# Kernel tuning notes

Hardware: AMD Instinct MI355X
Metric: run time of the kernel (lower is better)

Reference implementation:

```python
import jax, jax.numpy as jnp
import numpy as np

WS = 8        # window size (square)
HEADS = 8
DIM = 512
EPS = 1e-5


def _ln(x, g, b):
    m = x.mean(-1, keepdims=True)
    v = x.var(-1, keepdims=True)
    return (x - m) / jnp.sqrt(v + EPS) * g + b


def _bn(x, g, b, m, v):
    # eval-mode BatchNorm2d on NCHW
    sh = (1, -1, 1, 1)
    return (x - m.reshape(sh)) / jnp.sqrt(v.reshape(sh) + EPS) * g.reshape(sh) + b.reshape(sh)


def _win_rev(w, H, W, C):
    # (B*nW, WS*WS, C) -> (B, C, H, W)
    x = w.reshape(-1, H // WS, W // WS, WS, WS, C)
    return x.transpose(0, 5, 1, 3, 2, 4).reshape(-1, C, H, W)


def _win_part(x):
    # (B, C, H, W) -> (B*nW, WS*WS, C)
    B, C, H, W = x.shape
    x = x.reshape(B, C, H // WS, WS, W // WS, WS)
    return x.transpose(0, 2, 4, 3, 5, 1).reshape(-1, WS * WS, C)


def setup_inputs() -> dict:
    key = jax.random.key(0)
    ks = iter(jax.random.split(key, 64))
    def nrm(sh, s=0.02):
        return jax.random.normal(next(ks), sh, jnp.float32) * s
    C, C2, C8 = DIM, DIM // 2, DIM // 8
    B, H, W = 2, 224, 224
    N = WS * WS
    B_ = B * (H // WS) * (W // WS)
    # relative position index (same construction as the torch module)
    coords = np.stack(np.meshgrid(np.arange(WS), np.arange(WS), indexing='ij'))
    cf = coords.reshape(2, -1)
    rel = (cf[:, :, None] - cf[:, None, :]).transpose(1, 2, 0).astype(np.int64)
    rel[:, :, 0] += WS - 1
    rel[:, :, 1] += WS - 1
    rel[:, :, 0] *= 2 * WS - 1
    rel_idx = jnp.asarray(rel.sum(-1), jnp.int32)   # (N, N)
    ones = lambda n: jnp.ones((n,), jnp.float32)
    zeros = lambda n: jnp.zeros((n,), jnp.float32)
    return dict(
        x=jax.random.normal(next(ks), (B_, N, C), jnp.float32),
        w_pa=nrm((C, C2)), b_pa=zeros(C2),
        g_lna=ones(C2) + nrm((C2,), 0.1), b_lna=nrm((C2,), 0.1),
        w_pc=nrm((C, C)), b_pc=zeros(C),
        g_lnc=ones(C) + nrm((C,), 0.1), b_lnc=nrm((C,), 0.1),
        dw_w=nrm((C, 1, 3, 3), 0.1), dw_b=zeros(C),
        g_bn1=ones(C), b_bn1=zeros(C), m_bn1=nrm((C,), 0.1), v_bn1=ones(C),
        ci_w1=nrm((C, C8)), ci_b1=zeros(C8),
        g_bn2=ones(C8), b_bn2=zeros(C8), m_bn2=nrm((C8,), 0.1), v_bn2=ones(C8),
        ci_w2=nrm((C8, C2)), ci_b2=zeros(C2),
        pj_w=nrm((C, C2)), pj_b=zeros(C2),
        g_bn3=ones(C2), b_bn3=zeros(C2), m_bn3=nrm((C2,), 0.1), v_bn3=ones(C2),
        w_qkv=nrm((C2, 3 * C2)), b_qkv=zeros(3 * C2),
        si_w1=nrm((C2, C8)), si_b1=zeros(C8),
        g_bn4=ones(C8), b_bn4=zeros(C8), m_bn4=nrm((C8,), 0.1), v_bn4=ones(C8),
        si_w2=nrm((C8, 1)), si_b2=zeros(1),
        g_lno=ones(C2) + nrm((C2,), 0.1), b_lno=nrm((C2,), 0.1),
        w_out=nrm((C, C)), b_out=zeros(C),
        rpb=nrm(((2 * WS - 1) ** 2, HEADS)),
        rel_idx=rel_idx, H=H, W=W,
    )


def _forward(x, w_pa, b_pa, g_lna, b_lna, w_pc, b_pc, g_lnc, b_lnc,
             dw_w, dw_b, g_bn1, b_bn1, m_bn1, v_bn1,
             ci_w1, ci_b1, g_bn2, b_bn2, m_bn2, v_bn2, ci_w2, ci_b2,
             pj_w, pj_b, g_bn3, b_bn3, m_bn3, v_bn3,
             w_qkv, b_qkv,
             si_w1, si_b1, g_bn4, b_bn4, m_bn4, v_bn4, si_w2, si_b2,
             g_lno, b_lno, w_out, b_out, rpb, rel_idx, H, W):
    B_, N, C = x.shape
    C2 = C // 2
    hd = C2 // HEADS
    scale = hd ** -0.5
    x_att = _ln(x @ w_pa + b_pa, g_lna, b_lna)            # (B_, N, C2)
    x_cnn = _ln(x @ w_pc + b_pc, g_lnc, b_lnc)            # (B_, N, C)
    x_cnn = _win_rev(x_cnn, H, W, C)                      # (B, C, H, W)
    # depthwise 3x3 conv + BN + GELU
    x_cnn = jax.lax.conv_general_dilated(
        x_cnn, dw_w, (1, 1), [(1, 1), (1, 1)],
        feature_group_count=C, dimension_numbers=('NCHW', 'OIHW', 'NCHW')
    ) + dw_b.reshape(1, -1, 1, 1)
    x_cnn = jax.nn.gelu(_bn(x_cnn, g_bn1, b_bn1, m_bn1, v_bn1), approximate=False)
    # channel interaction: global avg pool -> 1x1 conv -> BN -> GELU -> 1x1 conv
    ci = x_cnn.mean((2, 3))                               # (B, C)
    ci = ci @ ci_w1 + ci_b1                               # (B, C/8)
    ci = jax.nn.gelu((ci - m_bn2) / jnp.sqrt(v_bn2 + EPS) * g_bn2 + b_bn2, approximate=False)
    ci = ci @ ci_w2 + ci_b2                               # (B, C2)
    x_cnn = jnp.einsum('bchw,co->bohw', x_cnn, pj_w) + pj_b.reshape(1, -1, 1, 1)  # (B, C2, H, W)
    # windowed multi-head attention
    qkv = (x_att @ w_qkv + b_qkv).reshape(B_, N, 3, HEADS, hd).transpose(2, 0, 3, 1, 4)
    q, k, v = qkv[0], qkv[1], qkv[2]                      # (B_, heads, N, hd)
    B = ci.shape[0]
    gate = jax.nn.sigmoid(ci).reshape(B, 1, HEADS, 1, hd)
    v = (v.reshape(B, -1, HEADS, N, hd) * gate).reshape(B_, HEADS, N, hd)
    attn = jnp.einsum('bhnd,bhmd->bhnm', q * scale, k)    # (B_, heads, N, N)
    bias = rpb[rel_idx[:N, :N].reshape(-1)].reshape(N, N, HEADS).transpose(2, 0, 1)
    attn = jax.nn.softmax(attn + bias[None], axis=-1)
    x_att = jnp.einsum('bhnm,bhmd->bnhd', attn, v).reshape(B_, N, C2)
    # spatial interaction gating of the conv branch
    x_sp = _win_rev(x_att, H, W, C2)                      # (B, C2, H, W)
    si = jnp.einsum('bchw,co->bohw', x_sp, si_w1) + si_b1.reshape(1, -1, 1, 1)
    si = jax.nn.gelu(_bn(si, g_bn4, b_bn4, m_bn4, v_bn4), approximate=False)
    si = jnp.einsum('bchw,co->bohw', si, si_w2) + si_b2.reshape(1, -1, 1, 1)      # (B, 1, H, W)
    x_cnn = _bn(jax.nn.sigmoid(si) * x_cnn, g_bn3, b_bn3, m_bn3, v_bn3)
    x_cnn = _win_part(x_cnn)                              # (B_, N, C2)
    x_att = _ln(x_att, g_lno, b_lno)
    return jnp.concatenate([x_att, x_cnn], axis=-1) @ w_out + b_out


def reference(x, w_pa, b_pa, g_lna, b_lna, w_pc, b_pc, g_lnc, b_lnc,
              dw_w, dw_b, g_bn1, b_bn1, m_bn1, v_bn1,
              ci_w1, ci_b1, g_bn2, b_bn2, m_bn2, v_bn2, ci_w2, ci_b2,
              pj_w, pj_b, g_bn3, b_bn3, m_bn3, v_bn3,
              w_qkv, b_qkv,
              si_w1, si_b1, g_bn4, b_bn4, m_bn4, v_bn4, si_w2, si_b2,
              g_lno, b_lno, w_out, b_out, rpb, rel_idx, H, W):
    return _forward(x, w_pa, b_pa, g_lna, b_lna, w_pc, b_pc, g_lnc, b_lnc,
                    dw_w, dw_b, g_bn1, b_bn1, m_bn1, v_bn1,
                    ci_w1, ci_b1, g_bn2, b_bn2, m_bn2, v_bn2, ci_w2, ci_b2,
                    pj_w, pj_b, g_bn3, b_bn3, m_bn3, v_bn3,
                    w_qkv, b_qkv,
                    si_w1, si_b1, g_bn4, b_bn4, m_bn4, v_bn4, si_w2, si_b2,
                    g_lno, b_lno, w_out, b_out, rpb, rel_idx, H, W)
```

## Files before the change

### kernel.cpp

```cpp
#include <hip/hip_runtime.h>
#include <math.h>

#define EPS 1e-5f
#define MROWS 100352
#define NWIN  1568

typedef __attribute__((ext_vector_type(8))) short bf16x8;
typedef __attribute__((ext_vector_type(4))) float f32x4;

__device__ __forceinline__ unsigned short f2bf(float f) {
  unsigned u = __float_as_uint(f);
  u += 0x7fffu + ((u >> 16) & 1u);
  return (unsigned short)(u >> 16);
}
__device__ __forceinline__ float bf2f(unsigned short s) {
  return __uint_as_float(((unsigned)s) << 16);
}
__device__ __forceinline__ float gelu_exact(float x) {
  return 0.5f * x * (1.f + erff(x * 0.70710678118654752f));
}

#define GLOAD16(gp, lp)                                              \
  __builtin_amdgcn_global_load_lds(                                  \
      (const __attribute__((address_space(1))) void*)(gp),           \
      (__attribute__((address_space(3))) void*)(lp), 16, 0, 0)

__device__ __forceinline__ void xcd_map(int& bx, int& by) {
  const int nwg = gridDim.x * gridDim.y;
  int n = blockIdx.y * gridDim.x + blockIdx.x;
  int w = n;
  if ((nwg & 7) == 0) w = (n & 7) * (nwg >> 3) + (n >> 3);
  by = w / gridDim.x;
  bx = w - by * gridDim.x;
}

template <bool OUTBF>
__global__ __launch_bounds__(256) void gemm_bf16(
    const unsigned short* __restrict__ A, const unsigned short* __restrict__ Bt,
    const float* __restrict__ bias, void* __restrict__ Cout,
    int M, int N, int K) {
  __shared__ unsigned short As[128 * 32];
  __shared__ unsigned short Bs[128 * 32];
  const int tid = threadIdx.x;
  const int lane = tid & 63, wave = tid >> 6;
  const int wr = wave >> 1, wc = wave & 1;
  int bx, by;
  xcd_map(bx, by);
  const int row0 = by * 128, col0 = bx * 128;
  const int lrow = tid >> 2, loff = (tid & 3) * 8;
  f32x4 acc[4][4];
#pragma unroll
  for (int m = 0; m < 4; ++m)
#pragma unroll
    for (int n = 0; n < 4; ++n) acc[m][n] = (f32x4){0.f, 0.f, 0.f, 0.f};
  for (int k0 = 0; k0 < K; k0 += 32) {
    __syncthreads();
#pragma unroll
    for (int p = 0; p < 2; ++p) {
      int r = p * 64 + lrow;
      GLOAD16(&A[(size_t)(row0 + r) * K + k0 + loff], &As[r * 32 + loff]);
      GLOAD16(&Bt[(size_t)(col0 + r) * K + k0 + loff], &Bs[r * 32 + loff]);
    }
    __syncthreads();
    const int g8 = (lane >> 4) * 8, rl = lane & 15;
    bf16x8 af[4], bfr[4];
#pragma unroll
    for (int m = 0; m < 4; ++m)
      af[m] = *(const bf16x8*)&As[(wr * 64 + m * 16 + rl) * 32 + g8];
#pragma unroll
    for (int n = 0; n < 4; ++n)
      bfr[n] = *(const bf16x8*)&Bs[(wc * 64 + n * 16 + rl) * 32 + g8];
#pragma unroll
    for (int m = 0; m < 4; ++m)
#pragma unroll
      for (int n = 0; n < 4; ++n)
        acc[m][n] = __builtin_amdgcn_mfma_f32_16x16x32_bf16(af[m], bfr[n],
                                                            acc[m][n], 0, 0, 0);
  }
  const int crow = (lane >> 4) * 4, ccol = lane & 15;
#pragma unroll
  for (int n = 0; n < 4; ++n) {
    const int gc = col0 + wc * 64 + n * 16 + ccol;
    const float bz = bias[gc];
#pragma unroll
    for (int m = 0; m < 4; ++m) {
      const int gr0 = row0 + wr * 64 + m * 16 + crow;
#pragma unroll
      for (int r = 0; r < 4; ++r) {
        float val = acc[m][n][r] + bz;
        if constexpr (OUTBF)
          ((unsigned short*)Cout)[(size_t)(gr0 + r) * N + gc] = f2bf(val);
        else
          ((float*)Cout)[(size_t)(gr0 + r) * N + gc] = val;
      }
    }
  }
}

__global__ __launch_bounds__(256) void gemm_f32a(
    const float* __restrict__ A, const unsigned short* __restrict__ Bt,
    const float* __restrict__ bias, unsigned short* __restrict__ Cout,
    int M, int N, int K) {
  __shared__ unsigned short As[128 * 32];
  __shared__ unsigned short Bs[128 * 32];
  const int tid = threadIdx.x;
  const int lane = tid & 63, wave = tid >> 6;
  const int wr = wave >> 1, wc = wave & 1;
  int bx, by;
  xcd_map(bx, by);
  const int row0 = by * 128, col0 = bx * 128;
  const int lrow = tid >> 2, loff = (tid & 3) * 8;
  const int ar = tid >> 1, ac = (tid & 1) * 16;
  f32x4 acc[4][4];
#pragma unroll
  for (int m = 0; m < 4; ++m)
#pragma unroll
    for (int n = 0; n < 4; ++n) acc[m][n] = (f32x4){0.f, 0.f, 0.f, 0.f};
  for (int k0 = 0; k0 < K; k0 += 32) {
    float4 f[4];
#pragma unroll
    for (int i = 0; i < 4; ++i)
      f[i] = *(const float4*)&A[(size_t)(row0 + ar) * K + k0 + ac + i * 4];
    __syncthreads();
#pragma unroll
    for (int p = 0; p < 2; ++p) {
      int r = p * 64 + lrow;
      GLOAD16(&Bt[(size_t)(col0 + r) * K + k0 + loff], &Bs[r * 32 + loff]);
    }
#pragma unroll
    for (int i = 0; i < 4; ++i) {
      unsigned p0, p1;
      asm("v_cvt_pk_bf16_f32 %0, %1, %2" : "=v"(p0) : "v"(f[i].x), "v"(f[i].y));
      asm("v_cvt_pk_bf16_f32 %0, %1, %2" : "=v"(p1) : "v"(f[i].z), "v"(f[i].w));
      *(uint2*)&As[ar * 32 + ac + i * 4] = make_uint2(p0, p1);
    }
    __syncthreads();
    const int g8 = (lane >> 4) * 8, rl = lane & 15;
    bf16x8 af[4], bfr[4];
#pragma unroll
    for (int m = 0; m < 4; ++m)
      af[m] = *(const bf16x8*)&As[(wr * 64 + m * 16 + rl) * 32 + g8];
#pragma unroll
    for (int n = 0; n < 4; ++n)
      bfr[n] = *(const bf16x8*)&Bs[(wc * 64 + n * 16 + rl) * 32 + g8];
#pragma unroll
    for (int m = 0; m < 4; ++m)
#pragma unroll
      for (int n = 0; n < 4; ++n)
        acc[m][n] = __builtin_amdgcn_mfma_f32_16x16x32_bf16(af[m], bfr[n],
                                                            acc[m][n], 0, 0, 0);
  }
  const int crow = (lane >> 4) * 4, ccol = lane & 15;
#pragma unroll
  for (int n = 0; n < 4; ++n) {
    const int gc = col0 + wc * 64 + n * 16 + ccol;
    const float bz = bias[gc];
#pragma unroll
    for (int m = 0; m < 4; ++m) {
      const int gr0 = row0 + wr * 64 + m * 16 + crow;
#pragma unroll
      for (int r = 0; r < 4; ++r)
        Cout[(size_t)(gr0 + r) * N + gc] = f2bf(acc[m][n][r] + bz);
    }
  }
}

__global__ __launch_bounds__(256) void wt_convert(const float* __restrict__ in,
                                                  unsigned short* __restrict__ out,
                                                  int K, int N) {
  int i = blockIdx.x * 256 + threadIdx.x;
  if (i >= K * N) return;
  int n = i / K, k = i - n * K;
  out[i] = f2bf(in[(size_t)k * N + n]);
}

__global__ __launch_bounds__(256) void pack_bias(const float* __restrict__ b_pa,
                                                 const float* __restrict__ b_pc,
                                                 float* __restrict__ out) {
  int t = blockIdx.x * 256 + threadIdx.x;
  if (t < 256) out[t] = b_pa[t];
  else if (t < 768) out[t] = b_pc[t - 256];
}

template <int W>
__global__ __launch_bounds__(256) void ln_rows_bf(
    const unsigned short* __restrict__ in, int istride,
    unsigned short* __restrict__ out,
    const float* __restrict__ g, const float* __restrict__ b) {
  const int row = blockIdx.x * 4 + (threadIdx.x >> 6);
  const int t = threadIdx.x & 63;
  constexpr int NE = W / 64;
  float v[NE];
  const size_t ibase = (size_t)row * istride + t * NE;
  const size_t obase = (size_t)row * W + t * NE;
#pragma unroll
  for (int c4 = 0; c4 < NE / 4; ++c4) {
    ushort4 u = *(const ushort4*)&in[ibase + c4 * 4];
    v[c4 * 4 + 0] = bf2f(u.x); v[c4 * 4 + 1] = bf2f(u.y);
    v[c4 * 4 + 2] = bf2f(u.z); v[c4 * 4 + 3] = bf2f(u.w);
  }
  float s = 0.f, sq = 0.f;
#pragma unroll
  for (int j = 0; j < NE; ++j) { s += v[j]; sq += v[j] * v[j]; }
#pragma unroll
  for (int off = 32; off >= 1; off >>= 1) {
    s += __shfl_xor(s, off);
    sq += __shfl_xor(sq, off);
  }
  const float mean = s * (1.f / W);
  const float var = sq * (1.f / W) - mean * mean;
  const float rstd = rsqrtf(var + EPS);
#pragma unroll
  for (int c4 = 0; c4 < NE / 4; ++c4) {
    int c = t * NE + c4 * 4;
    ushort4 o = make_ushort4(
        f2bf((v[c4 * 4 + 0] - mean) * rstd * g[c + 0] + b[c + 0]),
        f2bf((v[c4 * 4 + 1] - mean) * rstd * g[c + 1] + b[c + 1]),
        f2bf((v[c4 * 4 + 2] - mean) * rstd * g[c + 2] + b[c + 2]),
        f2bf((v[c4 * 4 + 3] - mean) * rstd * g[c + 3] + b[c + 3]));
    *(ushort4*)&out[obase + c4 * 4] = o;
  }
}

__global__ __launch_bounds__(256) void dwconv_bn_gelu(
    const unsigned short* __restrict__ xin, const float* __restrict__ wgt9,
    const float* __restrict__ dwb, const float* __restrict__ g1,
    const float* __restrict__ b1, const float* __restrict__ m1,
    const float* __restrict__ v1, unsigned short* __restrict__ outp,
    float* __restrict__ ci_part) {
  __shared__ unsigned short tile[100 * 128];
  __shared__ float psum[8 * 128];
  const int b_ = blockIdx.x;
  const int b = b_ / 784, win = b_ % 784;
  const int wi = win / 28, wj = win % 28;
  const int h0 = wi * 8 - 1, w0 = wj * 8 - 1;
  const int tid = threadIdx.x;
  const int c4 = (tid & 31) * 4;
  const int pg = tid >> 5;
  for (int chunk = 0; chunk < 4; ++chunk) {
    const int c0 = chunk * 128;
    __syncthreads();
#pragma unroll
    for (int it = 0; it < 7; ++it) {
      int idx = it * 256 + tid;
      if (idx < 1600) {
        int p = idx >> 4;
        int ch8 = (idx & 15) * 8;
        int ph = h0 + p / 10, pw = w0 + p % 10;
        uint4 val = {0u, 0u, 0u, 0u};
        if (ph >= 0 && ph < 224 && pw >= 0 && pw < 224) {
          int bs = b * 784 + (ph >> 3) * 28 + (pw >> 3);
          int n = ((ph & 7) << 3) | (pw & 7);
          val = *(const uint4*)&xin[(size_t)(bs * 64 + n) * 512 + c0 + ch8];
        }
        *(uint4*)&tile[p * 128 + ch8] = val;
      }
    }
    __syncthreads();
    float wreg[9][4];
    float scale[4], shift[4], bias0[4];
#pragma unroll
    for (int j = 0; j < 4; ++j) {
      int cc = c0 + c4 + j;
#pragma unroll
      for (int k = 0; k < 9; ++k) wreg[k][j] = wgt9[cc * 9 + k];
      scale[j] = g1[cc] * rsqrtf(v1[cc] + EPS);
      shift[j] = b1[cc] - m1[cc] * scale[j];
      bias0[j] = dwb[cc];
    }
    float cs0 = 0.f, cs1 = 0.f, cs2 = 0.f, cs3 = 0.f;
    for (int q = 0; q < 8; ++q) {
      const int qq = pg * 8 + q;
      const int r = qq >> 3, cc_ = qq & 7;
      float a0 = bias0[0], a1 = bias0[1], a2 = bias0[2], a3 = bias0[3];
#pragma unroll
      for (int dr = 0; dr < 3; ++dr)
#pragma unroll
        for (int dc = 0; dc < 3; ++dc) {
          ushort4 u = *(const ushort4*)&tile[((r + dr) * 10 + cc_ + dc) * 128 + c4];
          const int k = dr * 3 + dc;
          a0 += bf2f(u.x) * wreg[k][0];
          a1 += bf2f(u.y) * wreg[k][1];
          a2 += bf2f(u.z) * wreg[k][2];
          a3 += bf2f(u.w) * wreg[k][3];
        }
      float g0 = gelu_exact(a0 * scale[0] + shift[0]);
      float g1v = gelu_exact(a1 * scale[1] + shift[1]);
      float g2v = gelu_exact(a2 * scale[2] + shift[2]);
      float g3v = gelu_exact(a3 * scale[3] + shift[3]);
      cs0 += g0; cs1 += g1v; cs2 += g2v; cs3 += g3v;
      *(ushort4*)&outp[(size_t)(b_ * 64 + qq) * 512 + c0 + c4] =
          make_ushort4(f2bf(g0), f2bf(g1v), f2bf(g2v), f2bf(g3v));
    }
    *(float4*)&psum[pg * 128 + c4] = make_float4(cs0, cs1, cs2, cs3);
    __syncthreads();
    if (tid < 128) {
      float s = 0.f;
#pragma unroll
      for (int g = 0; g < 8; ++g) s += psum[g * 128 + tid];
      ci_part[(size_t)b_ * 512 + c0 + tid] = s;
    }
  }
}

__global__ __launch_bounds__(512) void ci_reduce(const float* __restrict__ ci_part,
                                                 float* __restrict__ ci_mean) {
  const int b = blockIdx.x, c = threadIdx.x;
  float s = 0.f;
  for (int w = 0; w < 784; ++w) s += ci_part[(size_t)(b * 784 + w) * 512 + c];
  ci_mean[b * 512 + c] = s * (1.f / 50176.f);
}

__global__ __launch_bounds__(512) void ci_gate(
    const float* __restrict__ ci_mean, const float* __restrict__ w1,
    const float* __restrict__ bi1, const float* __restrict__ g2,
    const float* __restrict__ b2, const float* __restrict__ m2,
    const float* __restrict__ v2, const float* __restrict__ w2,
    const float* __restrict__ bi2, float* __restrict__ gate) {
  __shared__ float cm[1024];
  __shared__ float c1[128];
  const int t = threadIdx.x;
  cm[t] = ci_mean[t];
  cm[t + 512] = ci_mean[t + 512];
  __syncthreads();
  if (t < 128) {
    int b = t >> 6, j = t & 63;
    float acc = bi1[j];
    for (int c = 0; c < 512; ++c) acc += cm[b * 512 + c] * w1[c * 64 + j];
    float sc = g2[j] * rsqrtf(v2[j] + EPS);
    c1[t] = gelu_exact((acc - m2[j]) * sc + b2[j]);
  }
  __syncthreads();
  {
    int b = t >> 8, o = t & 255;
    float acc = bi2[o];
#pragma unroll
    for (int j = 0; j < 64; ++j) acc += c1[b * 64 + j] * w2[j * 256 + o];
    gate[b * 256 + o] = 1.f / (1.f + expf(-acc));
  }
}

__global__ __launch_bounds__(256) void bias_pre(const float* __restrict__ rpb,
                                                const int* __restrict__ rel,
                                                float* __restrict__ biasf) {
  int i = blockIdx.x * 256 + threadIdx.x;
  if (i >= 4096) return;
  int r = rel[i];
#pragma unroll
  for (int h = 0; h < 8; ++h) biasf[h * 4096 + i] = rpb[r * 8 + h];
}

__global__ __launch_bounds__(256) void attn_mfma(
    const unsigned short* __restrict__ qkv,
    const float* __restrict__ gate,
    const float* __restrict__ biasf,
    unsigned short* __restrict__ outp) {
  __shared__ unsigned short lds[4 * (64 * 68 + 32 * 68)];
  const int w = blockIdx.x;
  const int b = w / 784;
  const int tid = threadIdx.x, lane = tid & 63, wave = tid >> 6;
  unsigned short* p_lds = lds + wave * (64 * 68 + 32 * 68);
  unsigned short* vT = p_lds + 64 * 68;
  const int l15 = lane & 15, l4 = lane >> 4;
  const float scale = 0.17677669529663687f;
  for (int hh = 0; hh < 2; ++hh) {
    const int h = wave * 2 + hh;
    {
      const float* gh = &gate[b * 256 + h * 32];
      const size_t vbase = ((size_t)w * 64 + lane) * 768 + 512 + h * 32;
#pragma unroll
      for (int c = 0; c < 4; ++c) {
        uint4 vv = *(const uint4*)&qkv[vbase + c * 8];
        float4 gA = *(const float4*)&gh[c * 8];
        float4 gB = *(const float4*)&gh[c * 8 + 4];
        unsigned vw[4] = {vv.x, vv.y, vv.z, vv.w};
        float gg[8] = {gA.x, gA.y, gA.z, gA.w, gB.x, gB.y, gB.z, gB.w};
#pragma unroll
        for (int j = 0; j < 4; ++j) {
          int d = c * 8 + j * 2;
          vT[(d + 0) * 68 + lane] = f2bf(__uint_as_float(vw[j] << 16) * gg[j * 2]);
          vT[(d + 1) * 68 + lane] =
              f2bf(__uint_as_float(vw[j] & 0xffff0000u) * gg[j * 2 + 1]);
        }
      }
    }
    bf16x8 kf[4], qf[4];
    const size_t qkbase = (size_t)w * 64 * 768 + h * 32 + l4 * 8;
#pragma unroll
    for (int t = 0; t < 4; ++t) {
      kf[t] = *(const bf16x8*)&qkv[qkbase + (size_t)(t * 16 + l15) * 768 + 256];
      qf[t] = *(const bf16x8*)&qkv[qkbase + (size_t)(t * 16 + l15) * 768];
    }
    f32x4 s[4][4];
#pragma unroll
    for (int mt = 0; mt < 4; ++mt)
#pragma unroll
      for (int nt = 0; nt < 4; ++nt) s[mt][nt] = (f32x4){0.f, 0.f, 0.f, 0.f};
#pragma unroll
    for (int mt = 0; mt < 4; ++mt)
#pragma unroll
      for (int nt = 0; nt < 4; ++nt)
        s[mt][nt] = __builtin_amdgcn_mfma_f32_16x16x32_bf16(kf[mt], qf[nt],
                                                            s[mt][nt], 0, 0, 0);
    float inv_s[4];
#pragma unroll
    for (int nt = 0; nt < 4; ++nt) {
      float mx = -1e30f;
#pragma unroll
      for (int mt = 0; mt < 4; ++mt) {
        float4 b4 = *(const float4*)&biasf[(h * 64 + nt * 16 + l15) * 64 +
                                           mt * 16 + l4 * 4];
        s[mt][nt][0] = s[mt][nt][0] * scale + b4.x;
        s[mt][nt][1] = s[mt][nt][1] * scale + b4.y;
        s[mt][nt][2] = s[mt][nt][2] * scale + b4.z;
        s[mt][nt][3] = s[mt][nt][3] * scale + b4.w;
#pragma unroll
        for (int r = 0; r < 4; ++r) mx = fmaxf(mx, s[mt][nt][r]);
      }
      mx = fmaxf(mx, __shfl_xor(mx, 16));
      mx = fmaxf(mx, __shfl_xor(mx, 32));
      float sum = 0.f;
#pragma unroll
      for (int mt = 0; mt < 4; ++mt)
#pragma unroll
        for (int r = 0; r < 4; ++r) {
          float e = __expf(s[mt][nt][r] - mx);
          s[mt][nt][r] = e;
          sum += e;
        }
      sum += __shfl_xor(sum, 16);
      sum += __shfl_xor(sum, 32);
      inv_s[nt] = 1.f / sum;
    }
#pragma unroll
    for (int nt = 0; nt < 4; ++nt)
#pragma unroll
      for (int mt = 0; mt < 4; ++mt) {
        ushort4 pk = make_ushort4(f2bf(s[mt][nt][0] * inv_s[nt]),
                                  f2bf(s[mt][nt][1] * inv_s[nt]),
                                  f2bf(s[mt][nt][2] * inv_s[nt]),
                                  f2bf(s[mt][nt][3] * inv_s[nt]));
        *(ushort4*)&p_lds[(nt * 16 + l15) * 68 + mt * 16 + l4 * 4] = pk;
      }
    f32x4 o[4][2];
#pragma unroll
    for (int i = 0; i < 4; ++i)
#pragma unroll
      for (int dt = 0; dt < 2; ++dt) o[i][dt] = (f32x4){0.f, 0.f, 0.f, 0.f};
#pragma unroll
    for (int ks = 0; ks < 2; ++ks) {
      bf16x8 pa[4], vf[2];
#pragma unroll
      for (int i = 0; i < 4; ++i) {
        const unsigned short* pp = &p_lds[(i * 16 + l15) * 68 + ks * 32 + l4 * 8];
        union { bf16x8 v; ushort4 u[2]; } tmp;
        tmp.u[0] = *(const ushort4*)pp;
        tmp.u[1] = *(const ushort4*)(pp + 4);
        pa[i] = tmp.v;
      }
#pragma unroll
      for (int dt = 0; dt < 2; ++dt) {
        const unsigned short* vp = &vT[(dt * 16 + l15) * 68 + ks * 32 + l4 * 8];
        union { bf16x8 v; ushort4 u[2]; } tmp;
        tmp.u[0] = *(const ushort4*)vp;
        tmp.u[1] = *(const ushort4*)(vp + 4);
        vf[dt] = tmp.v;
      }
#pragma unroll
      for (int i = 0; i < 4; ++i)
#pragma unroll
        for (int dt = 0; dt < 2; ++dt)
          o[i][dt] = __builtin_amdgcn_mfma_f32_16x16x32_bf16(pa[i], vf[dt],
                                                             o[i][dt], 0, 0, 0);
    }
#pragma unroll
    for (int i = 0; i < 4; ++i)
#pragma unroll
      for (int dt = 0; dt < 2; ++dt)
#pragma unroll
        for (int r = 0; r < 4; ++r)
          outp[((size_t)w * 64 + i * 16 + l4 * 4 + r) * 256 + h * 32 +
               dt * 16 + l15] = f2bf(o[i][dt][r]);
  }
}

__global__ __launch_bounds__(256) void si_ln_concat(
    const unsigned short* __restrict__ xatt, const unsigned short* __restrict__ xpj,
    const float* __restrict__ w1, const float* __restrict__ bi1,
    const float* __restrict__ g4, const float* __restrict__ b4v,
    const float* __restrict__ m4, const float* __restrict__ v4,
    const float* __restrict__ w2, const float* __restrict__ bi2,
    const float* __restrict__ g3, const float* __restrict__ b3v,
    const float* __restrict__ m3, const float* __restrict__ v3,
    const float* __restrict__ glno, const float* __restrict__ blno,
    unsigned short* __restrict__ outc) {
  __shared__ float xr[16 * 256];
  __shared__ float s1s[16 * 64];
  __shared__ float sig[16];
  const int t = threadIdx.x;
  const int row0 = blockIdx.x * 16;
#pragma unroll
  for (int i = 0; i < 2; ++i) {
    int idx = i * 256 + t;
    int pr = idx >> 5, pc = (idx & 31) * 8;
    const unsigned short* src = &xatt[(size_t)(row0 + pr) * 256 + pc];
    ushort4 a = *(const ushort4*)src;
    ushort4 c = *(const ushort4*)(src + 4);
    float* dst = &xr[pr * 256 + pc];
    dst[0] = bf2f(a.x); dst[1] = bf2f(a.y); dst[2] = bf2f(a.z); dst[3] = bf2f(a.w);
    dst[4] = bf2f(c.x); dst[5] = bf2f(c.y); dst[6] = bf2f(c.z); dst[7] = bf2f(c.w);
  }
  __syncthreads();
  {
    const int j = t & 63, pg = t >> 6;
    float acc[4];
    const float bj = bi1[j];
#pragma unroll
    for (int i = 0; i < 4; ++i) acc[i] = bj;
    for (int cc = 0; cc < 256; ++cc) {
      float wv = w1[cc * 64 + j];
#pragma unroll
      for (int i = 0; i < 4; ++i) acc[i] += xr[(pg * 4 + i) * 256 + cc] * wv;
    }
    const float sc4 = g4[j] * rsqrtf(v4[j] + EPS);
    const float m4j = m4[j], b4j = b4v[j];
#pragma unroll
    for (int i = 0; i < 4; ++i)
      s1s[(pg * 4 + i) * 64 + j] = gelu_exact((acc[i] - m4j) * sc4 + b4j);
  }
  __syncthreads();
  if (t < 16) {
    float a2 = bi2[0];
#pragma unroll
    for (int jj = 0; jj < 64; ++jj) a2 += s1s[t * 64 + jj] * w2[jj];
    sig[t] = 1.f / (1.f + expf(-a2));
  }
  __syncthreads();
  {
    const int p = t >> 4, l = t & 15;
    float4 v4s[4];
    float s = 0.f, sq = 0.f;
#pragma unroll
    for (int cq = 0; cq < 4; ++cq) {
      float4 x4 = *(const float4*)&xr[p * 256 + cq * 64 + l * 4];
      v4s[cq] = x4;
      s += x4.x + x4.y + x4.z + x4.w;
      sq += x4.x * x4.x + x4.y * x4.y + x4.z * x4.z + x4.w * x4.w;
    }
#pragma unroll
    for (int off = 8; off >= 1; off >>= 1) {
      s += __shfl_xor(s, off);
      sq += __shfl_xor(sq, off);
    }
    const float mean = s * (1.f / 256.f);
    const float var = sq * (1.f / 256.f) - mean * mean;
    const float rstd = rsqrtf(var + EPS);
    const size_t orow = (size_t)(row0 + p) * 512;
#pragma unroll
    for (int cq = 0; cq < 4; ++cq) {
      int c = cq * 64 + l * 4;
      float4 x4 = v4s[cq];
      *(ushort4*)&outc[orow + c] = make_ushort4(
          f2bf((x4.x - mean) * rstd * glno[c + 0] + blno[c + 0]),
          f2bf((x4.y - mean) * rstd * glno[c + 1] + blno[c + 1]),
          f2bf((x4.z - mean) * rstd * glno[c + 2] + blno[c + 2]),
          f2bf((x4.w - mean) * rstd * glno[c + 3] + blno[c + 3]));
    }
    const float sg = sig[p];
#pragma unroll
    for (int cq = 0; cq < 4; ++cq) {
      int c = cq * 64 + l * 4;
      ushort4 pu = *(const ushort4*)&xpj[(size_t)(row0 + p) * 256 + c];
      float px = bf2f(pu.x), py = bf2f(pu.y), pz = bf2f(pu.z), pw = bf2f(pu.w);
      float sc0 = g3[c + 0] * rsqrtf(v3[c + 0] + EPS);
      float sc1 = g3[c + 1] * rsqrtf(v3[c + 1] + EPS);
      float sc2 = g3[c + 2] * rsqrtf(v3[c + 2] + EPS);
      float sc3 = g3[c + 3] * rsqrtf(v3[c + 3] + EPS);
      *(ushort4*)&outc[orow + 256 + c] = make_ushort4(
          f2bf(sg * px * sc0 + (b3v[c + 0] - m3[c + 0] * sc0)),
          f2bf(sg * py * sc1 + (b3v[c + 1] - m3[c + 1] * sc1)),
          f2bf(sg * pz * sc2 + (b3v[c + 2] - m3[c + 2] * sc2)),
          f2bf(sg * pw * sc3 + (b3v[c + 3] - m3[c + 3] * sc3)));
    }
  }
}

extern "C" void kernel_launch(void* const* d_in, const int* in_sizes, int n_in,
                              void* d_out, int out_size, void* d_ws, size_t ws_size,
                              hipStream_t stream) {
  const float* x     = (const float*)d_in[0];
  const float* w_pa  = (const float*)d_in[1];
  const float* b_pa  = (const float*)d_in[2];
  const float* g_lna = (const float*)d_in[3];
  const float* b_lna = (const float*)d_in[4];
  const float* w_pc  = (const float*)d_in[5];
  const float* b_pc  = (const float*)d_in[6];
  const float* g_lnc = (const float*)d_in[7];
  const float* b_lnc = (const float*)d_in[8];
  const float* dw_w  = (const float*)d_in[9];
  const float* dw_b  = (const float*)d_in[10];
  const float* g_bn1 = (const float*)d_in[11];
  const float* b_bn1 = (const float*)d_in[12];
  const float* m_bn1 = (const float*)d_in[13];
  const float* v_bn1 = (const float*)d_in[14];
  const float* ci_w1 = (const float*)d_in[15];
  const float* ci_b1 = (const float*)d_in[16];
  const float* g_bn2 = (const float*)d_in[17];
  const float* b_bn2 = (const float*)d_in[18];
  const float* m_bn2 = (const float*)d_in[19];
  const float* v_bn2 = (const float*)d_in[20];
  const float* ci_w2 = (const float*)d_in[21];
  const float* ci_b2 = (const float*)d_in[22];
  const float* pj_w  = (const float*)d_in[23];
  const float* pj_b  = (const float*)d_in[24];
  const float* g_bn3 = (const float*)d_in[25];
  const float* b_bn3 = (const float*)d_in[26];
  const float* m_bn3 = (const float*)d_in[27];
  const float* v_bn3 = (const float*)d_in[28];
  const float* w_qkv = (const float*)d_in[29];
  const float* b_qkv = (const float*)d_in[30];
  const float* si_w1 = (const float*)d_in[31];
  const float* si_b1 = (const float*)d_in[32];
  const float* g_bn4 = (const float*)d_in[33];
  const float* b_bn4 = (const float*)d_in[34];
  const float* m_bn4 = (const float*)d_in[35];
  const float* v_bn4 = (const float*)d_in[36];
  const float* si_w2 = (const float*)d_in[37];
  const float* si_b2 = (const float*)d_in[38];
  const float* g_lno = (const float*)d_in[39];
  const float* b_lno = (const float*)d_in[40];
  const float* w_out = (const float*)d_in[41];
  const float* b_out = (const float*)d_in[42];
  const float* rpb   = (const float*)d_in[43];
  const int*   rel   = (const int*)d_in[44];

  char* ws = (char*)d_ws;
  unsigned short* G12BF = (unsigned short*)(ws + 0);
  unsigned short* QKVBF = (unsigned short*)(ws + 0);
  unsigned short* A1BF  = (unsigned short*)(ws + 154140672ull);
  unsigned short* ATTBF = (unsigned short*)(ws + 154140672ull);
  unsigned short* C1BF  = (unsigned short*)(ws + 205520896ull);
  unsigned short* CAT   = (unsigned short*)(ws + 205520896ull);
  unsigned short* CVBF  = (unsigned short*)(ws + 308281344ull);
  unsigned short* PJBF  = (unsigned short*)(ws + 411041792ull);
  float*          CIP   = (float*)(ws + 462422016ull);
  float*          CIM   = (float*)(ws + 465633280ull);
  float*          GATE  = (float*)(ws + 465637376ull);
  float*          B12   = (float*)(ws + 465639424ull);
  float*          BIASF = (float*)(ws + 465642496ull);
  unsigned short* WT    = (unsigned short*)(ws + 465773568ull);
  unsigned short* WpaT  = WT + 0;
  unsigned short* WpcT  = WT + 131072;
  unsigned short* PjT   = WT + 393216;
  unsigned short* QkvT  = WT + 524288;
  unsigned short* OutT  = WT + 720896;

  const int M = MROWS;
  dim3 b256(256), b512(512);

  wt_convert<<<512, b256, 0, stream>>>(w_pa, WpaT, 512, 256);
  wt_convert<<<1024, b256, 0, stream>>>(w_pc, WpcT, 512, 512);
  wt_convert<<<512, b256, 0, stream>>>(pj_w, PjT, 512, 256);
  wt_convert<<<768, b256, 0, stream>>>(w_qkv, QkvT, 256, 768);
  wt_convert<<<1024, b256, 0, stream>>>(w_out, OutT, 512, 512);
  pack_bias<<<3, b256, 0, stream>>>(b_pa, b_pc, B12);

  gemm_f32a<<<dim3(6, M / 128), b256, 0, stream>>>(x, WpaT, B12, G12BF, M, 768, 512);
  ln_rows_bf<256><<<M / 4, b256, 0, stream>>>(G12BF, 768, A1BF, g_lna, b_lna);
  ln_rows_bf<512><<<M / 4, b256, 0, stream>>>(G12BF + 256, 768, C1BF, g_lnc, b_lnc);

  dwconv_bn_gelu<<<NWIN, b256, 0, stream>>>(C1BF, dw_w, dw_b, g_bn1, b_bn1, m_bn1,
                                            v_bn1, CVBF, CIP);
  ci_reduce<<<2, b512, 0, stream>>>(CIP, CIM);
  ci_gate<<<1, b512, 0, stream>>>(CIM, ci_w1, ci_b1, g_bn2, b_bn2, m_bn2, v_bn2,
                                  ci_w2, ci_b2, GATE);
  bias_pre<<<16, b256, 0, stream>>>(rpb, rel, BIASF);

  gemm_bf16<true><<<dim3(2, M / 128), b256, 0, stream>>>(CVBF, PjT, pj_b, PJBF, M, 256, 512);

  gemm_bf16<true><<<dim3(6, M / 128), b256, 0, stream>>>(A1BF, QkvT, b_qkv, QKVBF, M, 768, 256);

  attn_mfma<<<NWIN, b256, 0, stream>>>(QKVBF, GATE, BIASF, ATTBF);

  si_ln_concat<<<M / 16, b256, 0, stream>>>(ATTBF, PJBF, si_w1, si_b1, g_bn4, b_bn4,
                                            m_bn4, v_bn4, si_w2, si_b2, g_bn3,
                                            b_bn3, m_bn3, v_bn3, g_lno, b_lno, CAT);

  gemm_bf16<false><<<dim3(4, M / 128), b256, 0, stream>>>(CAT, OutT, b_out,
                                                          (float*)d_out, M, 512, 512);
}
```

Before: 853.8 us.

## Double-buffer LDS tiles in bf16 GEMM kernels to overlap loads with MFMA

Both GEMM kernels now use two LDS buffers for the A and B tiles. The next K-slice is prefetched while MFMAs run on the current one, which leaves one barrier per iteration instead of two. In the f32-A kernel, the global loads of the next tile are issued before the math and converted into the alternate buffer afterwards, with the per-thread A layout changed to 4 rows by 8 columns. This doubles LDS use per block (32 KB) and raises register pressure, which may reduce occupancy.

```diff
diff --git a/kernel.cpp b/kernel.cpp
--- a/kernel.cpp
+++ b/kernel.cpp
@@ -39,8 +39,8 @@
     const unsigned short* __restrict__ A, const unsigned short* __restrict__ Bt,
     const float* __restrict__ bias, void* __restrict__ Cout,
     int M, int N, int K) {
-  __shared__ unsigned short As[128 * 32];
-  __shared__ unsigned short Bs[128 * 32];
+  __shared__ unsigned short As[2][128 * 32];
+  __shared__ unsigned short Bs[2][128 * 32];
   const int tid = threadIdx.x;
   const int lane = tid & 63, wave = tid >> 6;
   const int wr = wave >> 1, wc = wave & 1;
@@ -48,28 +48,51 @@
   xcd_map(bx, by);
   const int row0 = by * 128, col0 = bx * 128;
   const int lrow = tid >> 2, loff = (tid & 3) * 8;
+  const int g8 = (lane >> 4) * 8, rl = lane & 15;
   f32x4 acc[4][4];
 #pragma unroll
   for (int m = 0; m < 4; ++m)
 #pragma unroll
     for (int n = 0; n < 4; ++n) acc[m][n] = (f32x4){0.f, 0.f, 0.f, 0.f};
-  for (int k0 = 0; k0 < K; k0 += 32) {
-    __syncthreads();
+#pragma unroll
+  for (int p = 0; p < 2; ++p) {
+    int r = p * 64 + lrow;
+    GLOAD16(&A[(size_t)(row0 + r) * K + loff], &As[0][r * 32 + loff]);
+    GLOAD16(&Bt[(size_t)(col0 + r) * K + loff], &Bs[0][r * 32 + loff]);
+  }
+  __syncthreads();
+  int cur = 0;
+  for (int k0 = 32; k0 < K; k0 += 32) {
 #pragma unroll
     for (int p = 0; p < 2; ++p) {
       int r = p * 64 + lrow;
-      GLOAD16(&A[(size_t)(row0 + r) * K + k0 + loff], &As[r * 32 + loff]);
-      GLOAD16(&Bt[(size_t)(col0 + r) * K + k0 + loff], &Bs[r * 32 + loff]);
-    }
+      GLOAD16(&A[(size_t)(row0 + r) * K + k0 + loff], &As[cur ^ 1][r * 32 + loff]);
+      GLOAD16(&Bt[(size_t)(col0 + r) * K + k0 + loff], &Bs[cur ^ 1][r * 32 + loff]);
+    }
+    bf16x8 af[4], bfr[4];
+#pragma unroll
+    for (int m = 0; m < 4; ++m)
+      af[m] = *(const bf16x8*)&As[cur][(wr * 64 + m * 16 + rl) * 32 + g8];
+#pragma unroll
+    for (int n = 0; n < 4; ++n)
+      bfr[n] = *(const bf16x8*)&Bs[cur][(wc * 64 + n * 16 + rl) * 32 + g8];
+#pragma unroll
+    for (int m = 0; m < 4; ++m)
+#pragma unroll
+      for (int n = 0; n < 4; ++n)
+        acc[m][n] = __builtin_amdgcn_mfma_f32_16x16x32_bf16(af[m], bfr[n],
+                                                            acc[m][n], 0, 0, 0);
     __syncthreads();
-    const int g8 = (lane >> 4) * 8, rl = lane & 15;
+    cur ^= 1;
+  }
+  {
     bf16x8 af[4], bfr[4];
 #pragma unroll
     for (int m = 0; m < 4; ++m)
-      af[m] = *(const bf16x8*)&As[(wr * 64 + m * 16 + rl) * 32 + g8];
+      af[m] = *(const bf16x8*)&As[cur][(wr * 64 + m * 16 + rl) * 32 + g8];
 #pragma unroll
     for (int n = 0; n < 4; ++n)
-      bfr[n] = *(const bf16x8*)&Bs[(wc * 64 + n * 16 + rl) * 32 + g8];
+      bfr[n] = *(const bf16x8*)&Bs[cur][(wc * 64 + n * 16 + rl) * 32 + g8];
 #pragma unroll
     for (int m = 0; m < 4; ++m)
 #pragma unroll
@@ -101,8 +124,8 @@
     const float* __restrict__ A, const unsigned short* __restrict__ Bt,
     const float* __restrict__ bias, unsigned short* __restrict__ Cout,
     int M, int N, int K) {
-  __shared__ unsigned short As[128 * 32];
-  __shared__ unsigned short Bs[128 * 32];
+  __shared__ unsigned short As[2][128 * 32];
+  __shared__ unsigned short Bs[2][128 * 32];
   const int tid = threadIdx.x;
   const int lane = tid & 63, wave = tid >> 6;
   const int wr = wave >> 1, wc = wave & 1;
@@ -110,45 +133,86 @@
   xcd_map(bx, by);
   const int row0 = by * 128, col0 = bx * 128;
   const int lrow = tid >> 2, loff = (tid & 3) * 8;
-  const int ar = tid >> 1, ac = (tid & 1) * 16;
+  const int arow = tid >> 2, acol = (tid & 3) * 8;
+  const int g8 = (lane >> 4) * 8, rl = lane & 15;
   f32x4 acc[4][4];
 #pragma unroll
   for (int m = 0; m < 4; ++m)
 #pragma unroll
     for (int n = 0; n < 4; ++n) acc[m][n] = (f32x4){0.f, 0.f, 0.f, 0.f};
-  for (int k0 = 0; k0 < K; k0 += 32) {
-    float4 f[4];
-#pragma unroll
-    for (int i = 0; i < 4; ++i)
-      f[i] = *(const float4*)&A[(size_t)(row0 + ar) * K + k0 + ac + i * 4];
-    __syncthreads();
+
+#define LOADA(k0, f00, f01, f10, f11)                                          \
+  f00 = *(const float4*)&A[(size_t)(row0 + arow) * K + (k0) + acol];           \
+  f01 = *(const float4*)&A[(size_t)(row0 + arow) * K + (k0) + acol + 4];       \
+  f10 = *(const float4*)&A[(size_t)(row0 + arow + 64) * K + (k0) + acol];      \
+  f11 = *(const float4*)&A[(size_t)(row0 + arow + 64) * K + (k0) + acol + 4];
+
+#define WRITEA(buf, f00, f01, f10, f11)                                        \
+  {                                                                            \
+    unsigned q0, q1, q2, q3;                                                   \
+    asm("v_cvt_pk_bf16_f32 %0, %1, %2" : "=v"(q0) : "v"(f00.x), "v"(f00.y));   \
+    asm("v_cvt_pk_bf16_f32 %0, %1, %2" : "=v"(q1) : "v"(f00.z), "v"(f00.w));   \
+    asm("v_cvt_pk_bf16_f32 %0, %1, %2" : "=v"(q2) : "v"(f01.x), "v"(f01.y));   \
+    asm("v_cvt_pk_bf16_f32 %0, %1, %2" : "=v"(q3) : "v"(f01.z), "v"(f01.w));   \
+    *(uint4*)&As[buf][arow * 32 + acol] = make_uint4(q0, q1, q2, q3);          \
+    asm("v_cvt_pk_bf16_f32 %0, %1, %2" : "=v"(q0) : "v"(f10.x), "v"(f10.y));   \
+    asm("v_cvt_pk_bf16_f32 %0, %1, %2" : "=v"(q1) : "v"(f10.z), "v"(f10.w));   \
+    asm("v_cvt_pk_bf16_f32 %0, %1, %2" : "=v"(q2) : "v"(f11.x), "v"(f11.y));   \
+    asm("v_cvt_pk_bf16_f32 %0, %1, %2" : "=v"(q3) : "v"(f11.z), "v"(f11.w));   \
+    *(uint4*)&As[buf][(arow + 64) * 32 + acol] = make_uint4(q0, q1, q2, q3);   \
+  }
+
+  {
+    float4 f00, f01, f10, f11;
+    LOADA(0, f00, f01, f10, f11);
 #pragma unroll
     for (int p = 0; p < 2; ++p) {
       int r = p * 64 + lrow;
-      GLOAD16(&Bt[(size_t)(col0 + r) * K + k0 + loff], &Bs[r * 32 + loff]);
-    }
-#pragma unroll
-    for (int i = 0; i < 4; ++i) {
-      unsigned p0, p1;
-      asm("v_cvt_pk_bf16_f32 %0, %1, %2" : "=v"(p0) : "v"(f[i].x), "v"(f[i].y));
-      asm("v_cvt_pk_bf16_f32 %0, %1, %2" : "=v"(p1) : "v"(f[i].z), "v"(f[i].w));
-      *(uint2*)&As[ar * 32 + ac + i * 4] = make_uint2(p0, p1);
-    }
-    __syncthreads();
-    const int g8 = (lane >> 4) * 8, rl = lane & 15;
+      GLOAD16(&Bt[(size_t)(col0 + r) * K + loff], &Bs[0][r * 32 + loff]);
+    }
+    WRITEA(0, f00, f01, f10, f11);
+  }
+  __syncthreads();
+  int cur = 0;
+  for (int k0 = 32; k0 < K; k0 += 32) {
+    float4 f00, f01, f10, f11;
+    LOADA(k0, f00, f01, f10, f11);
+#pragma unroll
+    for (int p = 0; p < 2; ++p) {
+      int r = p * 64 + lrow;
+      GLOAD16(&Bt[(size_t)(col0 + r) * K + k0 + loff], &Bs[cur ^ 1][r * 32 + loff]);
+    }
     bf16x8 af[4], bfr[4];
 #pragma unroll
     for (int m = 0; m < 4; ++m)
-      af[m] = *(const bf16x8*)&As[(wr * 64 + m * 16 + rl) * 32 + g8];
+      af[m] = *(const bf16x8*)&As[cur][(wr * 64 + m * 16 + rl) * 32 + g8];
 #pragma unroll
     for (int n = 0; n < 4; ++n)
-      bfr[n] = *(const bf16x8*)&Bs[(wc * 64 + n * 16 + rl) * 32 + g8];
+      bfr[n] = *(const bf16x8*)&Bs[cur][(wc * 64 + n * 16 + rl) * 32 + g8];
 #pragma unroll
     for (int m = 0; m < 4; ++m)
 #pragma unroll
       for (int n = 0; n < 4; ++n)
         acc[m][n] = __builtin_amdgcn_mfma_f32_16x16x32_bf16(af[m], bfr[n],
                                                             acc[m][n], 0, 0, 0);
+    WRITEA(cur ^ 1, f00, f01, f10, f11);
+    __syncthreads();
+    cur ^= 1;
+  }
+  {
+    bf16x8 af[4], bfr[4];
+#pragma unroll
+    for (int m = 0; m < 4; ++m)
+      af[m] = *(const bf16x8*)&As[cur][(wr * 64 + m * 16 + rl) * 32 + g8];
+#pragma unroll
+    for (int n = 0; n < 4; ++n)
+      bfr[n] = *(const bf16x8*)&Bs[cur][(wc * 64 + n * 16 + rl) * 32 + g8];
+#pragma unroll
+    for (int m = 0; m < 4; ++m)
+#pragma unroll
+      for (int n = 0; n < 4; ++n)
+        acc[m][n] = __builtin_amdgcn_mfma_f32_16x16x32_bf16(af[m], bfr[n],
+                                                            acc[m][n], 0, 0, 0);
   }
   const int crow = (lane >> 4) * 4, ccol = lane & 15;
 #pragma unroll
@@ -163,6 +227,8 @@
         Cout[(size_t)(gr0 + r) * N + gc] = f2bf(acc[m][n][r] + bz);
     }
   }
+#undef LOADA
+#undef WRITEA
 }
 
 __global__ __launch_bounds__(256) void wt_convert(const float* __restrict__ in,
```

Result: no change. 844.6 us (-1.1%).
